# Performance work log

Measured on AMD Instinct MI355X. Metric: run time of the kernel, lower is better.

## Reference

```python
import jax, jax.numpy as jnp
import numpy as np

DIM = 64  # per-head key dim; temp = sqrt(DIM)
B, S = 32, 2048  # flattened batch*heads, seq_len


def setup_inputs() -> dict:
    key = jax.random.key(0)
    kq, kk, kv = jax.random.split(key, 3)
    q = jax.random.normal(kq, (B, S, DIM), dtype=jnp.float32)
    k = jax.random.normal(kk, (B, S, DIM), dtype=jnp.float32)
    v = jax.random.normal(kv, (B, S, DIM), dtype=jnp.float32)
    return {"q": q, "k": k, "v": v}


def reference(q, k, v):
    temp = np.sqrt(DIM).astype(np.float32)
    # attn = bmm(q, k^T) / sqrt(dim): [B, Sq, Sk]
    attn = jnp.einsum("bqd,bkd->bqk", q, k) / temp
    # softmax over key dim (the view/softmax(dim=1)/view trick == softmax over last axis)
    attn = jax.nn.softmax(attn, axis=-1)
    # dropout p=0.0 -> identity
    out = jnp.einsum("bqk,bkd->bqd", attn, v)
    return out
```

## Files before the change

### kernel.cpp

```cpp
#include <hip/hip_runtime.h>
#include <hip/hip_bf16.h>

#define S_ 2048
#define D_ 64
#define BM 128
#define BN 128
#define KSTR 72
#define VSTR 136

typedef __attribute__((ext_vector_type(8))) short bf16x8;
typedef __attribute__((ext_vector_type(16))) float f32x16;

__device__ __forceinline__ unsigned int cvtpk(float lo, float hi) {
    unsigned int r;
    asm("v_cvt_pk_bf16_f32 %0, %1, %2" : "=v"(r) : "v"(lo), "v"(hi));
    return r;
}

__global__ __launch_bounds__(256, 2) void fattn(const float* __restrict__ q,
                                                const float* __restrict__ kg,
                                                const float* __restrict__ vg,
                                                float* __restrict__ out) {
    __shared__ ushort Kt[BN * KSTR];
    __shared__ ushort Vs[BN * KSTR];
    __shared__ ushort Vt[D_ * VSTR];

    const int tid  = threadIdx.x;
    const int wid  = tid >> 6;
    const int lane = tid & 63;
    const int lq   = lane & 31;
    const int lh   = lane >> 5;

    const int bid   = blockIdx.x;
    const int xcd   = bid & 7;
    const int slot  = bid >> 3;
    const int batch = xcd + 8 * (slot >> 4);
    const int qtile = slot & 15;

    const float* qp = q  + (size_t)batch * S_ * D_;
    const float* kp = kg + (size_t)batch * S_ * D_;
    const float* vp = vg + (size_t)batch * S_ * D_;

    const float SC = 0.18033688011112042f;
    const int qrow = qtile * BM + wid * 32 + lq;
    bf16x8 qf[4];
    {
        const float* qr = qp + (size_t)qrow * D_ + 8 * lh;
#pragma unroll
        for (int kk = 0; kk < 4; ++kk) {
            union { bf16x8 v; unsigned int u[4]; } uq;
#pragma unroll
            for (int j = 0; j < 4; ++j)
                uq.u[j] = cvtpk(qr[kk * 16 + 2 * j] * SC, qr[kk * 16 + 2 * j + 1] * SC);
            qf[kk] = uq.v;
        }
    }

    f32x16 O[2];
#pragma unroll
    for (int md = 0; md < 2; ++md)
#pragma unroll
        for (int j = 0; j < 16; ++j) O[md][j] = 0.f;
    float m = -INFINITY, l = 0.f;

    for (int kt = 0; kt < S_; kt += BN) {
        __syncthreads();
        {
            const float* ksrc = kp + (size_t)kt * D_;
            const float* vsrc = vp + (size_t)kt * D_;
#pragma unroll
            for (int p = 0; p < 4; ++p) {
                const int c = p * 256 + tid;
                const float4 a  = *(const float4*)(ksrc + c * 8);
                const float4 b  = *(const float4*)(ksrc + c * 8 + 4);
                uint4 ok;
                ok.x = cvtpk(a.x, a.y); ok.y = cvtpk(a.z, a.w);
                ok.z = cvtpk(b.x, b.y); ok.w = cvtpk(b.z, b.w);
                *(uint4*)(&Kt[(c >> 3) * KSTR + (c & 7) * 8]) = ok;
                const float4 va = *(const float4*)(vsrc + c * 8);
                const float4 vb = *(const float4*)(vsrc + c * 8 + 4);
                uint4 ov;
                ov.x = cvtpk(va.x, va.y); ov.y = cvtpk(va.z, va.w);
                ov.z = cvtpk(vb.x, vb.y); ov.w = cvtpk(vb.z, vb.w);
                *(uint4*)(&Vs[(c >> 3) * KSTR + (c & 7) * 8]) = ov;
            }
        }
        __syncthreads();

        f32x16 sa[4];
#pragma unroll
        for (int mt = 0; mt < 4; ++mt) {
            const ushort* krow = &Kt[(mt * 32 + lq) * KSTR + 8 * lh];
            f32x16 acc;
#pragma unroll
            for (int j = 0; j < 16; ++j) acc[j] = 0.f;
#pragma unroll
            for (int kk = 0; kk < 4; ++kk) {
                const bf16x8 kf = *(const bf16x8*)(krow + kk * 16);
                acc = __builtin_amdgcn_mfma_f32_32x32x16_bf16(kf, qf[kk], acc, 0, 0, 0);
            }
            sa[mt] = acc;
        }

        {
            const int d = tid & 63;
#pragma unroll
            for (int j = 0; j < 4; ++j) {
                const int chunk = (tid >> 6) + 4 * j;
                const ushort* src = &Vs[(chunk * 8) * KSTR + d];
                const unsigned int x0 = src[0 * KSTR], x1 = src[1 * KSTR];
                const unsigned int x2 = src[2 * KSTR], x3 = src[3 * KSTR];
                const unsigned int x4 = src[4 * KSTR], x5 = src[5 * KSTR];
                const unsigned int x6 = src[6 * KSTR], x7 = src[7 * KSTR];
                uint4 o;
                o.x = x0 | (x1 << 16); o.y = x2 | (x3 << 16);
                o.z = x4 | (x5 << 16); o.w = x6 | (x7 << 16);
                *(uint4*)(&Vt[d * VSTR + chunk * 8]) = o;
            }
        }

        float tg[4];
#pragma unroll
        for (int g = 0; g < 4; ++g) {
            float a  = fmaxf(sa[g][0], sa[g][1]);
            float b  = fmaxf(sa[g][2], sa[g][3]);
            float c  = fmaxf(sa[g][4], sa[g][5]);
            float d0 = fmaxf(sa[g][6], sa[g][7]);
            float e  = fmaxf(sa[g][8], sa[g][9]);
            float f  = fmaxf(sa[g][10], sa[g][11]);
            float h  = fmaxf(sa[g][12], sa[g][13]);
            float i  = fmaxf(sa[g][14], sa[g][15]);
            a = fmaxf(a, b); c = fmaxf(c, d0); e = fmaxf(e, f); h = fmaxf(h, i);
            tg[g] = fmaxf(fmaxf(a, c), fmaxf(e, h));
        }
        float tm = fmaxf(fmaxf(tg[0], tg[1]), fmaxf(tg[2], tg[3]));
        tm = fmaxf(tm, __shfl_xor(tm, 32, 64));
        const float mnew = fmaxf(m, tm);
        const float alpha = __builtin_amdgcn_exp2f(m - mnew);

        float r0 = 0.f, r1 = 0.f, r2 = 0.f, r3 = 0.f;
#pragma unroll
        for (int g = 0; g < 4; ++g)
#pragma unroll
            for (int j = 0; j < 16; j += 4) {
                const float e0 = __builtin_amdgcn_exp2f(sa[g][j]     - mnew);
                const float e1 = __builtin_amdgcn_exp2f(sa[g][j + 1] - mnew);
                const float e2 = __builtin_amdgcn_exp2f(sa[g][j + 2] - mnew);
                const float e3 = __builtin_amdgcn_exp2f(sa[g][j + 3] - mnew);
                sa[g][j] = e0; sa[g][j + 1] = e1; sa[g][j + 2] = e2; sa[g][j + 3] = e3;
                r0 += e0; r1 += e1; r2 += e2; r3 += e3;
            }
        float rs = (r0 + r1) + (r2 + r3);
        rs += __shfl_xor(rs, 32, 64);
        l = l * alpha + rs;
        m = mnew;
#pragma unroll
        for (int md = 0; md < 2; ++md)
#pragma unroll
            for (int j = 0; j < 16; ++j) O[md][j] *= alpha;

        __syncthreads();

#pragma unroll
        for (int g = 0; g < 4; ++g) {
#pragma unroll
            for (int h = 0; h < 2; ++h) {
                union { bf16x8 v; unsigned int u[4]; } pf;
#pragma unroll
                for (int i = 0; i < 4; ++i)
                    pf.u[i] = cvtpk(sa[g][h * 8 + 2 * i], sa[g][h * 8 + 2 * i + 1]);
                const int koff = g * 32 + h * 16 + 4 * lh;
#pragma unroll
                for (int md = 0; md < 2; ++md) {
                    const ushort* vb = &Vt[(md * 32 + lq) * VSTR + koff];
                    union { bf16x8 v; uint2 p[2]; } vf;
                    vf.p[0] = *(const uint2*)(vb);
                    vf.p[1] = *(const uint2*)(vb + 8);
                    O[md] = __builtin_amdgcn_mfma_f32_32x32x16_bf16(vf.v, pf.v, O[md], 0, 0, 0);
                }
            }
        }
    }

    const float linv = 1.0f / l;
    float* op = out + (size_t)batch * S_ * D_ + (size_t)qrow * D_;
#pragma unroll
    for (int md = 0; md < 2; ++md) {
#pragma unroll
        for (int r4 = 0; r4 < 4; ++r4) {
            const int d = md * 32 + r4 * 8 + 4 * lh;
            float4 st;
            st.x = O[md][r4 * 4 + 0] * linv;
            st.y = O[md][r4 * 4 + 1] * linv;
            st.z = O[md][r4 * 4 + 2] * linv;
            st.w = O[md][r4 * 4 + 3] * linv;
            *(float4*)(op + d) = st;
        }
    }
}

extern "C" void kernel_launch(void* const* d_in, const int* in_sizes, int n_in,
                              void* d_out, int out_size, void* d_ws, size_t ws_size,
                              hipStream_t stream) {
    const float* q = (const float*)d_in[0];
    const float* k = (const float*)d_in[1];
    const float* v = (const float*)d_in[2];
    float* o = (float*)d_out;

    fattn<<<dim3(512), dim3(256), 0, stream>>>(q, k, v, o);
}
```

Measured before the change: 137.5 us.

## Prefetch next K/V tile into registers while computing the current tile

The first K/V tile is now loaded and converted to bf16 before the main loop. Inside the loop, each iteration issues global loads for the next tile into registers before the QK^T and PV MFMA work, then converts and stores them to shared memory after the PV step. This hides global-load latency behind compute and removes one barrier per iteration. The cost is 64 extra live VGPRs per thread, which may cause spills or lower occupancy under the 2-blocks-per-CU launch bound.

```diff
diff --git a/kernel.cpp b/kernel.cpp
--- a/kernel.cpp
+++ b/kernel.cpp
@@ -63,29 +63,41 @@
         for (int j = 0; j < 16; ++j) O[md][j] = 0.f;
     float m = -INFINITY, l = 0.f;
 
+#pragma unroll
+    for (int p = 0; p < 4; ++p) {
+        const int c = p * 256 + tid;
+        const float4 a = *(const float4*)(kp + c * 8);
+        const float4 b = *(const float4*)(kp + c * 8 + 4);
+        uint4 ok;
+        ok.x = cvtpk(a.x, a.y); ok.y = cvtpk(a.z, a.w);
+        ok.z = cvtpk(b.x, b.y); ok.w = cvtpk(b.z, b.w);
+        *(uint4*)(&Kt[(c >> 3) * KSTR + (c & 7) * 8]) = ok;
+        const float4 x = *(const float4*)(vp + c * 8);
+        const float4 y = *(const float4*)(vp + c * 8 + 4);
+        uint4 ov;
+        ov.x = cvtpk(x.x, x.y); ov.y = cvtpk(x.z, x.w);
+        ov.z = cvtpk(y.x, y.y); ov.w = cvtpk(y.z, y.w);
+        *(uint4*)(&Vs[(c >> 3) * KSTR + (c & 7) * 8]) = ov;
+    }
+
+    float4 ka[4], kb[4], va[4], vb[4];
+
     for (int kt = 0; kt < S_; kt += BN) {
         __syncthreads();
-        {
-            const float* ksrc = kp + (size_t)kt * D_;
-            const float* vsrc = vp + (size_t)kt * D_;
+        const bool more = (kt + BN < S_);
+
+        if (more) {
+            const float* ks = kp + (size_t)(kt + BN) * D_;
+            const float* vs = vp + (size_t)(kt + BN) * D_;
 #pragma unroll
             for (int p = 0; p < 4; ++p) {
-                const int c = p * 256 + tid;
-                const float4 a  = *(const float4*)(ksrc + c * 8);
-                const float4 b  = *(const float4*)(ksrc + c * 8 + 4);
-                uint4 ok;
-                ok.x = cvtpk(a.x, a.y); ok.y = cvtpk(a.z, a.w);
-                ok.z = cvtpk(b.x, b.y); ok.w = cvtpk(b.z, b.w);
-                *(uint4*)(&Kt[(c >> 3) * KSTR + (c & 7) * 8]) = ok;
-                const float4 va = *(const float4*)(vsrc + c * 8);
-                const float4 vb = *(const float4*)(vsrc + c * 8 + 4);
-                uint4 ov;
-                ov.x = cvtpk(va.x, va.y); ov.y = cvtpk(va.z, va.w);
-                ov.z = cvtpk(vb.x, vb.y); ov.w = cvtpk(vb.z, vb.w);
-                *(uint4*)(&Vs[(c >> 3) * KSTR + (c & 7) * 8]) = ov;
-            }
-        }
-        __syncthreads();
+                const int c8 = (p * 256 + tid) * 8;
+                ka[p] = *(const float4*)(ks + c8);
+                kb[p] = *(const float4*)(ks + c8 + 4);
+                va[p] = *(const float4*)(vs + c8);
+                vb[p] = *(const float4*)(vs + c8 + 4);
+            }
+        }
 
         f32x16 sa[4];
 #pragma unroll
@@ -172,12 +184,27 @@
                 const int koff = g * 32 + h * 16 + 4 * lh;
 #pragma unroll
                 for (int md = 0; md < 2; ++md) {
-                    const ushort* vb = &Vt[(md * 32 + lq) * VSTR + koff];
+                    const ushort* vb2 = &Vt[(md * 32 + lq) * VSTR + koff];
                     union { bf16x8 v; uint2 p[2]; } vf;
-                    vf.p[0] = *(const uint2*)(vb);
-                    vf.p[1] = *(const uint2*)(vb + 8);
+                    vf.p[0] = *(const uint2*)(vb2);
+                    vf.p[1] = *(const uint2*)(vb2 + 8);
                     O[md] = __builtin_amdgcn_mfma_f32_32x32x16_bf16(vf.v, pf.v, O[md], 0, 0, 0);
                 }
+            }
+        }
+
+        if (more) {
+#pragma unroll
+            for (int p = 0; p < 4; ++p) {
+                const int c = p * 256 + tid;
+                uint4 ok;
+                ok.x = cvtpk(ka[p].x, ka[p].y); ok.y = cvtpk(ka[p].z, ka[p].w);
+                ok.z = cvtpk(kb[p].x, kb[p].y); ok.w = cvtpk(kb[p].z, kb[p].w);
+                *(uint4*)(&Kt[(c >> 3) * KSTR + (c & 7) * 8]) = ok;
+                uint4 ov;
+                ov.x = cvtpk(va[p].x, va[p].y); ov.y = cvtpk(va[p].z, va[p].w);
+                ov.z = cvtpk(vb[p].x, vb[p].y); ov.w = cvtpk(vb[p].z, vb[p].w);
+                *(uint4*)(&Vs[(c >> 3) * KSTR + (c & 7) * 8]) = ov;
             }
         }
     }
```

Result: no change. 136.1 us (-1.0%).
